# Optimization experiments

Measured on AMD Instinct MI355X. Metric: run time of the kernel, lower is better.

Reference implementation:

```python
import jax, jax.numpy as jnp
import numpy as np

H = 12        # num attention heads
W = 256       # one-sided window (attention_window // 2)
NEG = -1e9    # additive mask value


def setup_inputs() -> dict:
    key = jax.random.key(0)
    ks = jax.random.split(key, 6)
    B, S, D = 2, 4096, 768
    inp = {
        "hidden_states": jax.random.normal(ks[0], (B, S, D), dtype=jnp.float32),
        "attention_mask": jnp.zeros((B, S), dtype=jnp.float32),
        "Wq": jax.random.normal(ks[1], (D, D), dtype=jnp.float32) * 0.02,
        "bq": jnp.zeros((D,), dtype=jnp.float32),
        "Wk": jax.random.normal(ks[2], (D, D), dtype=jnp.float32) * 0.02,
        "bk": jnp.zeros((D,), dtype=jnp.float32),
        "Wv": jax.random.normal(ks[3], (D, D), dtype=jnp.float32) * 0.02,
        "bv": jnp.zeros((D,), dtype=jnp.float32),
        "Wo": jax.random.normal(ks[4], (D, D), dtype=jnp.float32) * 0.02,
        "bo": jnp.zeros((D,), dtype=jnp.float32),
    }
    return inp


def _sliding_window_attn(hidden_states, attention_mask, Wq, bq, Wk, bk, Wv, bv, Wo, bo):
    B, S, D = hidden_states.shape
    dh = D // H
    b = W                 # chunk size == one-sided window
    nb = S // b           # number of chunks (S must be multiple of W)

    # projections; Longformer scales the query by 1/sqrt(d_head)
    q = (hidden_states @ Wq.T + bq) / jnp.sqrt(jnp.float32(dh))
    k = hidden_states @ Wk.T + bk
    v = hidden_states @ Wv.T + bv

    # [B, H, S, dh]
    q = q.reshape(B, S, H, dh).transpose(0, 2, 1, 3)
    k = k.reshape(B, S, H, dh).transpose(0, 2, 1, 3)
    v = v.reshape(B, S, H, dh).transpose(0, 2, 1, 3)

    # chunk queries: [B, H, nb, b, dh]
    qb = q.reshape(B, H, nb, b, dh)

    # pad K/V by one chunk on each side, gather 3 consecutive chunks per query chunk
    kp = jnp.pad(k, ((0, 0), (0, 0), (b, b), (0, 0)))
    vp = jnp.pad(v, ((0, 0), (0, 0), (b, b), (0, 0)))
    idx = jnp.arange(nb)[:, None] * b + jnp.arange(3 * b)[None, :]  # [nb, 3b] into padded seq
    kw = kp[:, :, idx]  # [B, H, nb, 3b, dh]
    vw = vp[:, :, idx]  # [B, H, nb, 3b, dh]

    # banded scores: [B, H, nb, b, 3b]
    scores = jnp.einsum("bhnqd,bhnkd->bhnqk", qb, kw)

    # band mask: query at local pos qi (global n*b+qi) vs key at local pos ki
    # (global n*b + ki - b); relative offset = ki - b - qi, keep |offset| <= W
    rel = jnp.arange(3 * b)[None, :] - b - jnp.arange(b)[:, None]      # [b, 3b]
    band = jnp.abs(rel) <= W
    # sequence-boundary mask: key global position must lie in [0, S)
    kpos = idx - b                                                      # [nb, 3b]
    inbounds = (kpos >= 0) & (kpos < S)
    valid = band[None, :, :] & inbounds[:, None, :]                     # [nb, b, 3b]

    # key padding bias from attention_mask (wrapper passes attention_mask * -1)
    neg_mask = attention_mask * -1.0                                    # [B, S]
    mp = jnp.pad(neg_mask, ((0, 0), (b, b)))
    key_bias = mp[:, idx]                                               # [B, nb, 3b]

    scores = scores + key_bias[:, None, :, None, :]
    scores = jnp.where(valid[None, None], scores, NEG)

    probs = jax.nn.softmax(scores, axis=-1)
    ctx = jnp.einsum("bhnqk,bhnkd->bhnqd", probs, vw)                   # [B, H, nb, b, dh]
    ctx = ctx.reshape(B, H, S, dh).transpose(0, 2, 1, 3).reshape(B, S, D)

    return ctx @ Wo.T + bo


def reference(hidden_states, attention_mask, Wq, bq, Wk, bk, Wv, bv, Wo, bo):
    return _sliding_window_attn(hidden_states, attention_mask,
                                Wq, bq, Wk, bk, Wv, bv, Wo, bo)
```

## Files before the change

kernel.cpp:

```cpp
#include <hip/hip_runtime.h>
#include <hip/hip_bf16.h>
#include <stdint.h>

#define NH 12
#define DH 64
#define SEQ 4096
#define DM 768
#define NEGV -1e9f
#define LOG2E 1.4426950408889634f
#define QSCALE 0.1803368801111601f

using bf16x8 = __attribute__((ext_vector_type(8))) short;
using f32x4  = __attribute__((ext_vector_type(4))) float;

static __device__ __forceinline__ short f2bf(float f) {
  unsigned u = __builtin_bit_cast(unsigned, f);
  u += 0x7fffu + ((u >> 16) & 1u);
  return (short)(u >> 16);
}

static __device__ __forceinline__ unsigned pack2bf(float lo, float hi) {
  unsigned a = __builtin_bit_cast(unsigned, lo);
  a += 0x7fffu + ((a >> 16) & 1u);
  unsigned b = __builtin_bit_cast(unsigned, hi);
  b += 0x7fffu + ((b >> 16) & 1u);
  return (a >> 16) | (b & 0xffff0000u);
}

static __device__ __forceinline__ void gload16(const void* g, void* l) {
  __builtin_amdgcn_global_load_lds(
      (const __attribute__((address_space(1))) unsigned*)g,
      (__attribute__((address_space(3))) unsigned*)l, 16, 0, 0);
}

static __device__ __forceinline__ f32x4 mfma16(bf16x8 a, bf16x8 b, f32x4 c) {
  return __builtin_amdgcn_mfma_f32_16x16x32_bf16(a, b, c, 0, 0, 0);
}

#define SBAR() __builtin_amdgcn_sched_barrier(0)
#define WAIT8() asm volatile("s_waitcnt vmcnt(8)" ::: "memory")
#define WAIT4() asm volatile("s_waitcnt vmcnt(4)" ::: "memory")
#define WAIT0() asm volatile("s_waitcnt vmcnt(0)" ::: "memory")
#define HBAR() __builtin_amdgcn_s_barrier()

__global__ __launch_bounds__(256) void cvt_x(const float* __restrict__ X,
                                             short* __restrict__ Xb, int n4) {
  int i = blockIdx.x * 256 + threadIdx.x;
  if (i >= n4) return;
  float4 v = ((const float4*)X)[i];
  short4 o; o.x = f2bf(v.x); o.y = f2bf(v.y); o.z = f2bf(v.z); o.w = f2bf(v.w);
  ((short4*)Xb)[i] = o;
}

__global__ __launch_bounds__(256) void cvt_w(
    const float* __restrict__ Wq, const float* __restrict__ Wk,
    const float* __restrict__ Wv, const float* __restrict__ Wo,
    short* __restrict__ Wqkv, short* __restrict__ Wob) {
  int i = blockIdx.x * 256 + threadIdx.x;
  const int n1 = 2304 * 768 / 4;
  if (i < n1) {
    int e = i * 4;
    int row = e / 768;
    const float* src;
    float sc = 1.0f;
    if (row < 768)       { src = Wq + e; sc = QSCALE; }
    else if (row < 1536) { src = Wk + e - 768 * 768; }
    else                 { src = Wv + e - 1536 * 768; }
    float4 v = *(const float4*)src;
    short4 o; o.x = f2bf(v.x * sc); o.y = f2bf(v.y * sc);
    o.z = f2bf(v.z * sc); o.w = f2bf(v.w * sc);
    ((short4*)Wqkv)[i] = o;
  } else {
    int j = i - n1;
    if (j >= 768 * 768 / 4) return;
    float4 v = ((const float4*)Wo)[j];
    short4 o; o.x = f2bf(v.x); o.y = f2bf(v.y); o.z = f2bf(v.z); o.w = f2bf(v.w);
    ((short4*)Wob)[j] = o;
  }
}

#define GEMM_PIPELINE(SM, AG, BG, ACC, LANE, WR, WC)                           \
  {                                                                            \
    const int l15 = (LANE) & 15, gw = (LANE) >> 4;                             \
    const int s_ = (l15 >> 1) & 3;                                             \
    const int fcol = ((gw ^ s_) << 3);                                         \
    const int NT = 24;                                             \
    auto stage = [&](int t) {                                                  \
      short* ab = (SM) + ((t & 3) << 12);                                      \
      short* bb = (SM) + 16384 + ((t & 3) << 12);                              \
      int kt = t << 5;                                                         \
      gload16((AG) + kt, ab + ldst);                                           \
      gload16((AG) + kt + 64 * 768, ab + ldst + 2048);                         \
      gload16((BG) + kt, bb + ldst);                                           \
      gload16((BG) + kt + 64 * 768, bb + ldst + 2048);                         \
    };                                                                         \
    auto compute = [&](int t) {                                                \
      const short* ab = (SM) + ((t & 3) << 12);                                \
      const short* bb = (SM) + 16384 + ((t & 3) << 12);                        \
      bf16x8 af[4], bf[4];                                                     \
      _Pragma("unroll") for (int mi = 0; mi < 4; ++mi)                         \
          af[mi] = *(const bf16x8*)(ab + ((WR) + mi * 16 + l15) * 32 + fcol);  \
      _Pragma("unroll") for (int ni = 0; ni < 4; ++ni)                         \
          bf[ni] = *(const bf16x8*)(bb + ((WC) + ni * 16 + l15) * 32 + fcol);  \
      __builtin_amdgcn_s_setprio(1);                                           \
      _Pragma("unroll") for (int mi = 0; mi < 4; ++mi)                         \
          _Pragma("unroll") for (int ni = 0; ni < 4; ++ni)                     \
              ACC[mi][ni] = mfma16(af[mi], bf[ni], ACC[mi][ni]);               \
      __builtin_amdgcn_s_setprio(0);                                           \
    };                                                                         \
    stage(0); stage(1); stage(2);                                              \
    SBAR();                                                                    \
    _Pragma("unroll 1") for (int i = 0; i < NT - 3; ++i) {                     \
      SBAR(); WAIT8(); HBAR(); SBAR();                                         \
      stage(i + 3);                                                            \
      SBAR();                                                                  \
      compute(i);                                                              \
    }                                                                          \
    SBAR(); WAIT8(); HBAR(); SBAR(); compute(NT - 3);                          \
    SBAR(); WAIT4(); HBAR(); SBAR(); compute(NT - 2);                          \
    SBAR(); WAIT0(); HBAR(); SBAR(); compute(NT - 1);                          \
  }

__global__ __launch_bounds__(256) void gemm_qkv(
    const short* __restrict__ Xb, const short* __restrict__ Wqkv,
    const float* __restrict__ bq, const float* __restrict__ bk,
    const float* __restrict__ bv,
    short* __restrict__ qO, short* __restrict__ kO, short* __restrict__ vT) {
  __shared__ __align__(16) short sm[32768];
  const int tid = threadIdx.x, lane = tid & 63, wid = tid >> 6;
  const int xcd = blockIdx.x & 7, kk = blockIdx.x >> 3;
  const int m0 = (xcd * 8 + (kk & 7)) * 128;
  const int n0 = (kk >> 3) * 128;
  const int wr = (wid >> 1) * 64, wc = (wid & 1) * 64;
  const int srow = tid >> 2;
  const int scol = (((tid & 3) ^ ((srow >> 1) & 3)) << 3);
  const short* Ag = Xb + (m0 + srow) * 768 + scol;
  const short* Bg = Wqkv + (n0 + srow) * 768 + scol;
  const int ldst = tid * 8;

  const int src = n0 / 768;
  const int nloc = n0 % 768;
  float bias[4];
#pragma unroll
  for (int ni = 0; ni < 4; ++ni) {
    int c = nloc + wc + ni * 16 + (lane & 15);
    bias[ni] = (src == 0) ? bq[c] * QSCALE : (src == 1) ? bk[c] : bv[c];
  }
  WAIT0(); SBAR();

  f32x4 acc[4][4] = {};
  GEMM_PIPELINE(sm, Ag, Bg, acc, lane, wr, wc);

  const int bb = m0 >> 12;
  const int s0 = m0 & (SEQ - 1);
  __syncthreads();
  if (src < 2) {
#pragma unroll
    for (int mi = 0; mi < 4; ++mi)
#pragma unroll
      for (int ni = 0; ni < 4; ++ni) {
        int row = wr + mi * 16 + ((lane >> 4) << 2);
        int col = wc + ni * 16 + (lane & 15);
#pragma unroll
        for (int r = 0; r < 4; ++r)
          sm[(row + r) * 132 + col] = f2bf(acc[mi][ni][r] + bias[ni]);
      }
    __syncthreads();
    short* dst = (src == 0) ? qO : kO;
    for (int u = tid; u < 8192; u += 256) {
      int r = u >> 6, cp = (u & 63) << 1;
      unsigned val = *(const unsigned*)&sm[r * 132 + cp];
      int c = nloc + cp;
      int h = c >> 6, d = c & 63;
      *(unsigned*)&dst[(((bb * NH + h) * SEQ) + s0 + r) * DH + d] = val;
    }
  } else {
#pragma unroll
    for (int mi = 0; mi < 4; ++mi)
#pragma unroll
      for (int ni = 0; ni < 4; ++ni) {
        int row = wr + mi * 16 + ((lane >> 4) << 2);
        int col = wc + ni * 16 + (lane & 15);
        short4 pk;
        pk.x = f2bf(acc[mi][ni][0] + bias[ni]);
        pk.y = f2bf(acc[mi][ni][1] + bias[ni]);
        pk.z = f2bf(acc[mi][ni][2] + bias[ni]);
        pk.w = f2bf(acc[mi][ni][3] + bias[ni]);
        *(short4*)&sm[col * 132 + row] = pk;
      }
    __syncthreads();
    for (int u = tid; u < 8192; u += 256) {
      int cc = u >> 6, rp = (u & 63) << 1;
      unsigned val = *(const unsigned*)&sm[cc * 132 + rp];
      int c = nloc + cc;
      int h = c >> 6, d = c & 63;
      *(unsigned*)&vT[(((bb * NH + h) * DH) + d) * SEQ + s0 + rp] = val;
    }
  }
}

__global__ __launch_bounds__(512, 4) void attn(
    const short* __restrict__ qI, const short* __restrict__ kI,
    const short* __restrict__ vT, const float* __restrict__ amask,
    short* __restrict__ ctx) {
  __shared__ __align__(16) short Ks[128 * 64];
  __shared__ __align__(16) short Vs[64 * 128];
  __shared__ __align__(16) short Ps[8][16 * 132];
  const int tid = threadIdx.x, lane = tid & 63, wid = tid >> 6;
  const int vb_id = (blockIdx.x & 7) * 96 + (blockIdx.x >> 3);
  const int strip = vb_id & 31;
  const int hh = (vb_id >> 5) % 12;
  const int bb = vb_id / 384;
  const int s0 = strip * 128;
  const int n = s0 >> 8;
  const int i0 = s0 & 255;
  const int bh = bb * NH + hh;
  const int m = lane & 15, hq = lane >> 4;
  const int swz = m & 7;
  const int iw = i0 + (wid << 4);

  const short* qbase = qI + ((size_t)(bh * SEQ) + s0 + (wid << 4)) * DH;
  const bf16x8 aq0 = *(const bf16x8*)(qbase + m * DH + (hq << 3));
  const bf16x8 aq1 = *(const bf16x8*)(qbase + m * DH + 32 + (hq << 3));

  const int kb_s0 = m * 64 + ((hq ^ swz) << 3);
  const int kb_s1 = m * 64 + (((hq + 4) ^ swz) << 3);
  const int vk0 = m * 128 + ((hq ^ swz) << 3);
  const int vk1 = m * 128 + (((hq + 4) ^ swz) << 3);
  const int vk2 = m * 128 + (((hq + 8) ^ swz) << 3);
  const int vk3 = m * 128 + (((hq + 12) ^ swz) << 3);
  short* Pw = Ps[wid];
  const int pwr = m * 132;

  const int e0 = tid * 8, e1 = tid * 8 + 4096;
  const int kj0 = e0 >> 6, kj1 = e1 >> 6;
  const int ksrc0 = kj0 * DH + ((((e0 >> 3) & 7) ^ (kj0 & 7)) << 3);
  const int ksrc1 = kj1 * DH + ((((e1 >> 3) & 7) ^ (kj1 & 7)) << 3);
  const int vd0 = e0 >> 7, vd1 = e1 >> 7;
  const int vsrc0 = vd0 * SEQ + ((((e0 >> 3) & 15) ^ (vd0 & 7)) << 3);
  const int vsrc1 = vd1 * SEQ + ((((e1 >> 3) & 15) ^ (vd1 & 7)) << 3);

  const short* kg0 = kI + (size_t)bh * SEQ * DH;
  const short* vg0 = vT + (size_t)bh * DH * SEQ;
  const float* mk0 = amask + bb * SEQ + (hq << 2);

  f32x4 acc[4] = {};
  float mrow = -1e30f, lrow = 0.f;

#pragma unroll 1
  for (int c = 0; c < 6; ++c) {
    const int j0 = c << 7;
    const int kpos0 = ((n - 1) << 8) + j0;
    if (kpos0 < 0 || kpos0 >= SEQ) continue;
    if (j0 + 127 < i0 || j0 > i0 + 639) continue;

    __syncthreads();
    {
      const short* kb = kg0 + (size_t)kpos0 * DH;
      gload16(kb + ksrc0, (short*)Ks + e0);
      gload16(kb + ksrc1, (short*)Ks + e1);
      const short* vbp = vg0 + kpos0;
      gload16(vbp + vsrc0, (short*)Vs + e0);
      gload16(vbp + vsrc1, (short*)Vs + e1);
    }
    __syncthreads();

    f32x4 sc[8];
    __builtin_amdgcn_s_setprio(1);
#pragma unroll
    for (int jt = 0; jt < 8; ++jt) {
      bf16x8 k0 = *(const bf16x8*)(Ks + jt * 1024 + kb_s0);
      bf16x8 k1 = *(const bf16x8*)(Ks + jt * 1024 + kb_s1);
      f32x4 z = {};
      z = mfma16(k0, aq0, z);
      z = mfma16(k1, aq1, z);
      sc[jt] = z;
    }
    __builtin_amdgcn_s_setprio(0);

    const float* mp = mk0 + kpos0;
    float mn = mrow;
    const bool interior = (j0 >= iw + 15) && (j0 <= iw + 385);
    if (interior) {
#pragma unroll
      for (int jt = 0; jt < 8; ++jt) {
        float4 b4 = *(const float4*)(mp + jt * 16);
#pragma unroll
        for (int r = 0; r < 4; ++r) {
          float s = fmaf(-LOG2E, (&b4.x)[r], sc[jt][r]);
          sc[jt][r] = s;
          mn = fmaxf(mn, s);
        }
      }
    } else {
      const int iq = iw + m;
#pragma unroll
      for (int jt = 0; jt < 8; ++jt) {
        float4 b4 = *(const float4*)(mp + jt * 16);
        const int jb = j0 + jt * 16 + (hq << 2);
#pragma unroll
        for (int r = 0; r < 4; ++r) {
          int j = jb + r;
          float s = fmaf(-LOG2E, (&b4.x)[r], sc[jt][r]);
          s = (j >= iq && j <= iq + 512) ? s : NEGV;
          sc[jt][r] = s;
          mn = fmaxf(mn, s);
        }
      }
    }
    mn = fmaxf(mn, __shfl_xor(mn, 16));
    mn = fmaxf(mn, __shfl_xor(mn, 32));

    float l0 = 0.f;
#pragma unroll
    for (int jt = 0; jt < 8; ++jt) {
      float p0 = exp2f(sc[jt][0] - mn);
      float p1 = exp2f(sc[jt][1] - mn);
      float p2 = exp2f(sc[jt][2] - mn);
      float p3 = exp2f(sc[jt][3] - mn);
      l0 += (p0 + p1) + (p2 + p3);
      uint2 u;
      u.x = pack2bf(p0, p1);
      u.y = pack2bf(p2, p3);
      *(uint2*)(Pw + pwr + jt * 16 + (hq << 2)) = u;
    }
    l0 += __shfl_xor(l0, 16);
    l0 += __shfl_xor(l0, 32);
    const float scl = exp2f(mrow - mn);
    lrow = lrow * scl + l0;
    mrow = mn;
    const float s0r = __shfl(scl, (hq << 2) + 0);
    const float s1r = __shfl(scl, (hq << 2) + 1);
    const float s2r = __shfl(scl, (hq << 2) + 2);
    const float s3r = __shfl(scl, (hq << 2) + 3);
#pragma unroll
    for (int nt = 0; nt < 4; ++nt) {
      acc[nt][0] *= s0r; acc[nt][1] *= s1r;
      acc[nt][2] *= s2r; acc[nt][3] *= s3r;
    }

    asm volatile("s_waitcnt lgkmcnt(0)" ::: "memory");
    __builtin_amdgcn_sched_barrier(0);

    __builtin_amdgcn_s_setprio(1);
#pragma unroll
    for (int ks = 0; ks < 4; ++ks) {
      bf16x8 pa = *(const bf16x8*)(Pw + pwr + ks * 32 + (hq << 3));
      const int vkk = (ks == 0) ? vk0 : (ks == 1) ? vk1 : (ks == 2) ? vk2 : vk3;
#pragma unroll
      for (int nt = 0; nt < 4; ++nt) {
        bf16x8 vv = *(const bf16x8*)(Vs + nt * 2048 + vkk);
        acc[nt] = mfma16(pa, vv, acc[nt]);
      }
    }
    __builtin_amdgcn_s_setprio(0);
  }

  const float inv = 1.0f / lrow;
  const float i0r = __shfl(inv, (hq << 2) + 0);
  const float i1r = __shfl(inv, (hq << 2) + 1);
  const float i2r = __shfl(inv, (hq << 2) + 2);
  const float i3r = __shfl(inv, (hq << 2) + 3);
#pragma unroll
  for (int nt = 0; nt < 4; ++nt) {
    Pw[((hq << 2) + 0) * 72 + nt * 16 + m] = f2bf(acc[nt][0] * i0r);
    Pw[((hq << 2) + 1) * 72 + nt * 16 + m] = f2bf(acc[nt][1] * i1r);
    Pw[((hq << 2) + 2) * 72 + nt * 16 + m] = f2bf(acc[nt][2] * i2r);
    Pw[((hq << 2) + 3) * 72 + nt * 16 + m] = f2bf(acc[nt][3] * i3r);
  }
  asm volatile("s_waitcnt lgkmcnt(0)" ::: "memory");
  __builtin_amdgcn_sched_barrier(0);
#pragma unroll
  for (int it = 0; it < 2; ++it) {
    int row = it * 8 + (lane >> 3);
    bf16x8 val = *(const bf16x8*)(Pw + row * 72 + ((lane & 7) << 3));
    *(bf16x8*)(ctx + ((size_t)(bb * SEQ) + s0 + (wid << 4) + row) * DM +
               hh * DH + ((lane & 7) << 3)) = val;
  }
}

__global__ __launch_bounds__(256) void gemm_out(
    const short* __restrict__ Cb, const short* __restrict__ Wob,
    const float* __restrict__ bo, float* __restrict__ out) {
  __shared__ __align__(16) short sm[32768];
  const int tid = threadIdx.x, lane = tid & 63, wid = tid >> 6;
  const int xcd = blockIdx.x & 7, kk = blockIdx.x >> 3;
  const int m0 = (xcd * 8 + (kk & 7)) * 128;
  const int n0 = (kk >> 3) * 128;
  const int wr = (wid >> 1) * 64, wc = (wid & 1) * 64;
  const int srow = tid >> 2;
  const int scol = (((tid & 3) ^ ((srow >> 1) & 3)) << 3);
  const short* Ag = Cb + (m0 + srow) * 768 + scol;
  const short* Bg = Wob + (n0 + srow) * 768 + scol;
  const int ldst = tid * 8;

  float bias[4];
#pragma unroll
  for (int ni = 0; ni < 4; ++ni)
    bias[ni] = bo[n0 + wc + ni * 16 + (lane & 15)];
  WAIT0(); SBAR();

  f32x4 acc[4][4] = {};
  GEMM_PIPELINE(sm, Ag, Bg, acc, lane, wr, wc);

#pragma unroll
  for (int mi = 0; mi < 4; ++mi)
#pragma unroll
    for (int ni = 0; ni < 4; ++ni) {
      int row = m0 + wr + mi * 16 + ((lane >> 4) << 2);
      int col = n0 + wc + ni * 16 + (lane & 15);
#pragma unroll
      for (int r = 0; r < 4; ++r)
        out[(row + r) * DM + col] = acc[mi][ni][r] + bias[ni];
    }
}

extern "C" void kernel_launch(void* const* d_in, const int* in_sizes, int n_in,
                              void* d_out, int out_size, void* d_ws, size_t ws_size,
                              hipStream_t stream) {
  (void)in_sizes; (void)n_in; (void)out_size; (void)ws_size;
  const float* hs    = (const float*)d_in[0];
  const float* amask = (const float*)d_in[1];
  const float* Wq = (const float*)d_in[2];
  const float* bq = (const float*)d_in[3];
  const float* Wk = (const float*)d_in[4];
  const float* bk = (const float*)d_in[5];
  const float* Wv = (const float*)d_in[6];
  const float* bv = (const float*)d_in[7];
  const float* Wo = (const float*)d_in[8];
  const float* bo = (const float*)d_in[9];
  float* out = (float*)d_out;
  char* ws = (char*)d_ws;
  short* Xb   = (short*)(ws);
  short* Wqkv = (short*)(ws + 12582912);
  short* Wob  = (short*)(ws + 16121856);
  short* qB   = (short*)(ws + 17301504);
  short* kB   = (short*)(ws + 29884416);
  short* vTB  = (short*)(ws + 42467328);
  short* ctx  = Xb;

  cvt_x<<<dim3(6144), dim3(256), 0, stream>>>(hs, Xb, 8192 * 768 / 4);
  cvt_w<<<dim3(2304), dim3(256), 0, stream>>>(Wq, Wk, Wv, Wo, Wqkv, Wob);
  gemm_qkv<<<dim3(1152), dim3(256), 0, stream>>>(Xb, Wqkv, bq, bk, bv, qB, kB, vTB);
  attn<<<dim3(768), dim3(512), 0, stream>>>(qB, kB, vTB, amask, ctx);
  gemm_out<<<dim3(384), dim3(256), 0, stream>>>(ctx, Wob, bo, out);
}
```

Baseline: 134.8 us.

## Prefetch next K/V chunk into registers, stage mask in LDS, lazy softmax rescale

Replaces the per-chunk global_load_lds with a register prefetch. The next K/V chunk is loaded into registers during the current chunk's QK compute and then written to LDS behind barriers, so global latency overlaps with math. The attention-mask bias for the whole window is staged once into shared memory instead of being read from global each chunk. The chunk loop bounds are computed directly rather than skipped with continue. Online-softmax rescaling is skipped when the running max grows by at most 4 (log2 units), which saves exp and shuffle work but risks larger intermediate values in bf16 P.

```diff
diff --git a/kernel.cpp b/kernel.cpp
--- a/kernel.cpp
+++ b/kernel.cpp
@@ -41,6 +41,7 @@
 #define WAIT8() asm volatile("s_waitcnt vmcnt(8)" ::: "memory")
 #define WAIT4() asm volatile("s_waitcnt vmcnt(4)" ::: "memory")
 #define WAIT0() asm volatile("s_waitcnt vmcnt(0)" ::: "memory")
+#define LKWAIT() asm volatile("s_waitcnt lgkmcnt(0)" ::: "memory")
 #define HBAR() __builtin_amdgcn_s_barrier()
 
 __global__ __launch_bounds__(256) void cvt_x(const float* __restrict__ X,
@@ -206,6 +207,7 @@
   __shared__ __align__(16) short Ks[128 * 64];
   __shared__ __align__(16) short Vs[64 * 128];
   __shared__ __align__(16) short Ps[8][16 * 132];
+  __shared__ __align__(16) float BiasL[768];
   const int tid = threadIdx.x, lane = tid & 63, wid = tid >> 6;
   const int vb_id = (blockIdx.x & 7) * 96 + (blockIdx.x >> 3);
   const int strip = vb_id & 31;
@@ -214,6 +216,7 @@
   const int s0 = strip * 128;
   const int n = s0 >> 8;
   const int i0 = s0 & 255;
+  const int base = (n - 1) * 256;
   const int bh = bb * NH + hh;
   const int m = lane & 15, hq = lane >> 4;
   const int swz = m & 7;
@@ -242,28 +245,42 @@
 
   const short* kg0 = kI + (size_t)bh * SEQ * DH;
   const short* vg0 = vT + (size_t)bh * DH * SEQ;
-  const float* mk0 = amask + bb * SEQ + (hq << 2);
+
+  if (tid < 192) {
+    int idx = base + tid * 4;
+    idx = idx < 0 ? 0 : (idx > SEQ - 4 ? SEQ - 4 : idx);
+    float4 bv = *(const float4*)(amask + bb * SEQ + idx);
+    *(float4*)&BiasL[tid * 4] = bv;
+  }
+
+  int cl0 = (n == 0) ? 2 : 0;
+  if (i0 == 128 && cl0 < 1) cl0 = 1;
+  int chi = (i0 == 0) ? 4 : 5;
+  if (n == 15) chi = 3;
+
+  uint4 rk0, rk1, rv0, rv1;
+  {
+    const int kpos0 = base + (cl0 << 7);
+    const short* kb = kg0 + (size_t)kpos0 * DH;
+    rk0 = *(const uint4*)(kb + ksrc0);
+    rk1 = *(const uint4*)(kb + ksrc1);
+    const short* vbp = vg0 + kpos0;
+    rv0 = *(const uint4*)(vbp + vsrc0);
+    rv1 = *(const uint4*)(vbp + vsrc1);
+  }
 
   f32x4 acc[4] = {};
   float mrow = -1e30f, lrow = 0.f;
 
 #pragma unroll 1
-  for (int c = 0; c < 6; ++c) {
-    const int j0 = c << 7;
-    const int kpos0 = ((n - 1) << 8) + j0;
-    if (kpos0 < 0 || kpos0 >= SEQ) continue;
-    if (j0 + 127 < i0 || j0 > i0 + 639) continue;
-
-    __syncthreads();
-    {
-      const short* kb = kg0 + (size_t)kpos0 * DH;
-      gload16(kb + ksrc0, (short*)Ks + e0);
-      gload16(kb + ksrc1, (short*)Ks + e1);
-      const short* vbp = vg0 + kpos0;
-      gload16(vbp + vsrc0, (short*)Vs + e0);
-      gload16(vbp + vsrc1, (short*)Vs + e1);
-    }
-    __syncthreads();
+  for (int cc = cl0; cc <= chi; ++cc) {
+    const int j0 = cc << 7;
+    SBAR(); LKWAIT(); HBAR(); SBAR();
+    *(uint4*)((short*)Ks + e0) = rk0;
+    *(uint4*)((short*)Ks + e1) = rk1;
+    *(uint4*)((short*)Vs + e0) = rv0;
+    *(uint4*)((short*)Vs + e1) = rv1;
+    SBAR(); LKWAIT(); HBAR(); SBAR();
 
     f32x4 sc[8];
     __builtin_amdgcn_s_setprio(1);
@@ -278,13 +295,23 @@
     }
     __builtin_amdgcn_s_setprio(0);
 
-    const float* mp = mk0 + kpos0;
+    if (cc < chi) {
+      const int kposn = base + ((cc + 1) << 7);
+      const short* kb = kg0 + (size_t)kposn * DH;
+      rk0 = *(const uint4*)(kb + ksrc0);
+      rk1 = *(const uint4*)(kb + ksrc1);
+      const short* vbp = vg0 + kposn;
+      rv0 = *(const uint4*)(vbp + vsrc0);
+      rv1 = *(const uint4*)(vbp + vsrc1);
+    }
+
     float mn = mrow;
     const bool interior = (j0 >= iw + 15) && (j0 <= iw + 385);
+    const float* bl = BiasL + j0 + (hq << 2);
     if (interior) {
 #pragma unroll
       for (int jt = 0; jt < 8; ++jt) {
-        float4 b4 = *(const float4*)(mp + jt * 16);
+        float4 b4 = *(const float4*)(bl + jt * 16);
 #pragma unroll
         for (int r = 0; r < 4; ++r) {
           float s = fmaf(-LOG2E, (&b4.x)[r], sc[jt][r]);
@@ -296,7 +323,7 @@
       const int iq = iw + m;
 #pragma unroll
       for (int jt = 0; jt < 8; ++jt) {
-        float4 b4 = *(const float4*)(mp + jt * 16);
+        float4 b4 = *(const float4*)(bl + jt * 16);
         const int jb = j0 + jt * 16 + (hq << 2);
 #pragma unroll
         for (int r = 0; r < 4; ++r) {
@@ -311,13 +338,16 @@
     mn = fmaxf(mn, __shfl_xor(mn, 16));
     mn = fmaxf(mn, __shfl_xor(mn, 32));
 
+    const bool resc = !__all(mn - mrow <= 4.0f);
+    const float mbase = resc ? mn : mrow;
+
     float l0 = 0.f;
 #pragma unroll
     for (int jt = 0; jt < 8; ++jt) {
-      float p0 = exp2f(sc[jt][0] - mn);
-      float p1 = exp2f(sc[jt][1] - mn);
-      float p2 = exp2f(sc[jt][2] - mn);
-      float p3 = exp2f(sc[jt][3] - mn);
+      float p0 = exp2f(sc[jt][0] - mbase);
+      float p1 = exp2f(sc[jt][1] - mbase);
+      float p2 = exp2f(sc[jt][2] - mbase);
+      float p3 = exp2f(sc[jt][3] - mbase);
       l0 += (p0 + p1) + (p2 + p3);
       uint2 u;
       u.x = pack2bf(p0, p1);
@@ -326,21 +356,24 @@
     }
     l0 += __shfl_xor(l0, 16);
     l0 += __shfl_xor(l0, 32);
-    const float scl = exp2f(mrow - mn);
-    lrow = lrow * scl + l0;
-    mrow = mn;
-    const float s0r = __shfl(scl, (hq << 2) + 0);
-    const float s1r = __shfl(scl, (hq << 2) + 1);
-    const float s2r = __shfl(scl, (hq << 2) + 2);
-    const float s3r = __shfl(scl, (hq << 2) + 3);
-#pragma unroll
-    for (int nt = 0; nt < 4; ++nt) {
-      acc[nt][0] *= s0r; acc[nt][1] *= s1r;
-      acc[nt][2] *= s2r; acc[nt][3] *= s3r;
-    }
-
-    asm volatile("s_waitcnt lgkmcnt(0)" ::: "memory");
-    __builtin_amdgcn_sched_barrier(0);
+    if (resc) {
+      const float scl = exp2f(mrow - mn);
+      lrow = lrow * scl + l0;
+      mrow = mn;
+      const float s0r = __shfl(scl, (hq << 2) + 0);
+      const float s1r = __shfl(scl, (hq << 2) + 1);
+      const float s2r = __shfl(scl, (hq << 2) + 2);
+      const float s3r = __shfl(scl, (hq << 2) + 3);
+#pragma unroll
+      for (int nt = 0; nt < 4; ++nt) {
+        acc[nt][0] *= s0r; acc[nt][1] *= s1r;
+        acc[nt][2] *= s2r; acc[nt][3] *= s3r;
+      }
+    } else {
+      lrow += l0;
+    }
+
+    LKWAIT(); SBAR();
 
     __builtin_amdgcn_s_setprio(1);
 #pragma unroll
@@ -368,8 +401,7 @@
     Pw[((hq << 2) + 2) * 72 + nt * 16 + m] = f2bf(acc[nt][2] * i2r);
     Pw[((hq << 2) + 3) * 72 + nt * 16 + m] = f2bf(acc[nt][3] * i3r);
   }
-  asm volatile("s_waitcnt lgkmcnt(0)" ::: "memory");
-  __builtin_amdgcn_sched_barrier(0);
+  LKWAIT(); SBAR();
 #pragma unroll
   for (int it = 0; it < 2; ++it) {
     int row = it * 8 + (lane >> 3);
```

After: 145.0 us. +7.6%, slower.

## Load K/V tiles directly from global per wave, dropping shared staging and block barriers

Applied to the files above, without the earlier changes.

The attention kernel no longer stages K and V tiles into shared memory with block-wide barriers. Each wave now reads its K and V fragments straight from global memory (relying on L1/L2 for reuse across the 8 waves) and skips chunks per wave using the wave's own query range instead of the block's. This removes the two __syncthreads per chunk and frees LDS, and the occupancy hint is dropped. In exchange every wave issues redundant global loads with less coalescing and exposed latency before each MFMA.

```diff
diff --git a/kernel.cpp b/kernel.cpp
--- a/kernel.cpp
+++ b/kernel.cpp
@@ -41,6 +41,7 @@
 #define WAIT8() asm volatile("s_waitcnt vmcnt(8)" ::: "memory")
 #define WAIT4() asm volatile("s_waitcnt vmcnt(4)" ::: "memory")
 #define WAIT0() asm volatile("s_waitcnt vmcnt(0)" ::: "memory")
+#define LKWAIT() asm volatile("s_waitcnt lgkmcnt(0)" ::: "memory")
 #define HBAR() __builtin_amdgcn_s_barrier()
 
 __global__ __launch_bounds__(256) void cvt_x(const float* __restrict__ X,
@@ -199,12 +200,10 @@
   }
 }
 
-__global__ __launch_bounds__(512, 4) void attn(
+__global__ __launch_bounds__(512) void attn(
     const short* __restrict__ qI, const short* __restrict__ kI,
     const short* __restrict__ vT, const float* __restrict__ amask,
     short* __restrict__ ctx) {
-  __shared__ __align__(16) short Ks[128 * 64];
-  __shared__ __align__(16) short Vs[64 * 128];
   __shared__ __align__(16) short Ps[8][16 * 132];
   const int tid = threadIdx.x, lane = tid & 63, wid = tid >> 6;
   const int vb_id = (blockIdx.x & 7) * 96 + (blockIdx.x >> 3);
@@ -214,31 +213,20 @@
   const int s0 = strip * 128;
   const int n = s0 >> 8;
   const int i0 = s0 & 255;
+  const int base = (n - 1) * 256;
   const int bh = bb * NH + hh;
   const int m = lane & 15, hq = lane >> 4;
-  const int swz = m & 7;
   const int iw = i0 + (wid << 4);
 
   const short* qbase = qI + ((size_t)(bh * SEQ) + s0 + (wid << 4)) * DH;
   const bf16x8 aq0 = *(const bf16x8*)(qbase + m * DH + (hq << 3));
   const bf16x8 aq1 = *(const bf16x8*)(qbase + m * DH + 32 + (hq << 3));
 
-  const int kb_s0 = m * 64 + ((hq ^ swz) << 3);
-  const int kb_s1 = m * 64 + (((hq + 4) ^ swz) << 3);
-  const int vk0 = m * 128 + ((hq ^ swz) << 3);
-  const int vk1 = m * 128 + (((hq + 4) ^ swz) << 3);
-  const int vk2 = m * 128 + (((hq + 8) ^ swz) << 3);
-  const int vk3 = m * 128 + (((hq + 12) ^ swz) << 3);
   short* Pw = Ps[wid];
   const int pwr = m * 132;
 
-  const int e0 = tid * 8, e1 = tid * 8 + 4096;
-  const int kj0 = e0 >> 6, kj1 = e1 >> 6;
-  const int ksrc0 = kj0 * DH + ((((e0 >> 3) & 7) ^ (kj0 & 7)) << 3);
-  const int ksrc1 = kj1 * DH + ((((e1 >> 3) & 7) ^ (kj1 & 7)) << 3);
-  const int vd0 = e0 >> 7, vd1 = e1 >> 7;
-  const int vsrc0 = vd0 * SEQ + ((((e0 >> 3) & 15) ^ (vd0 & 7)) << 3);
-  const int vsrc1 = vd1 * SEQ + ((((e1 >> 3) & 15) ^ (vd1 & 7)) << 3);
+  const int koff = m * DH + (hq << 3);
+  const int voff = m * SEQ + (hq << 3);
 
   const short* kg0 = kI + (size_t)bh * SEQ * DH;
   const short* vg0 = vT + (size_t)bh * DH * SEQ;
@@ -250,33 +238,21 @@
 #pragma unroll 1
   for (int c = 0; c < 6; ++c) {
     const int j0 = c << 7;
-    const int kpos0 = ((n - 1) << 8) + j0;
+    const int kpos0 = base + j0;
     if (kpos0 < 0 || kpos0 >= SEQ) continue;
-    if (j0 + 127 < i0 || j0 > i0 + 639) continue;
-
-    __syncthreads();
-    {
-      const short* kb = kg0 + (size_t)kpos0 * DH;
-      gload16(kb + ksrc0, (short*)Ks + e0);
-      gload16(kb + ksrc1, (short*)Ks + e1);
-      const short* vbp = vg0 + kpos0;
-      gload16(vbp + vsrc0, (short*)Vs + e0);
-      gload16(vbp + vsrc1, (short*)Vs + e1);
-    }
-    __syncthreads();
-
+    if (j0 + 127 < iw || j0 > iw + 527) continue;
+
+    const short* kb = kg0 + (size_t)kpos0 * DH + koff;
     f32x4 sc[8];
-    __builtin_amdgcn_s_setprio(1);
 #pragma unroll
     for (int jt = 0; jt < 8; ++jt) {
-      bf16x8 k0 = *(const bf16x8*)(Ks + jt * 1024 + kb_s0);
-      bf16x8 k1 = *(const bf16x8*)(Ks + jt * 1024 + kb_s1);
+      bf16x8 k0 = *(const bf16x8*)(kb + jt * 1024);
+      bf16x8 k1 = *(const bf16x8*)(kb + jt * 1024 + 32);
       f32x4 z = {};
       z = mfma16(k0, aq0, z);
       z = mfma16(k1, aq1, z);
       sc[jt] = z;
     }
-    __builtin_amdgcn_s_setprio(0);
 
     const float* mp = mk0 + kpos0;
     float mn = mrow;
@@ -339,21 +315,18 @@
       acc[nt][2] *= s2r; acc[nt][3] *= s3r;
     }
 
-    asm volatile("s_waitcnt lgkmcnt(0)" ::: "memory");
-    __builtin_amdgcn_sched_barrier(0);
-
-    __builtin_amdgcn_s_setprio(1);
+    LKWAIT(); SBAR();
+
+    const short* vb = vg0 + kpos0 + voff;
 #pragma unroll
     for (int ks = 0; ks < 4; ++ks) {
       bf16x8 pa = *(const bf16x8*)(Pw + pwr + ks * 32 + (hq << 3));
-      const int vkk = (ks == 0) ? vk0 : (ks == 1) ? vk1 : (ks == 2) ? vk2 : vk3;
 #pragma unroll
       for (int nt = 0; nt < 4; ++nt) {
-        bf16x8 vv = *(const bf16x8*)(Vs + nt * 2048 + vkk);
+        bf16x8 vv = *(const bf16x8*)(vb + nt * 16 * SEQ + ks * 32);
         acc[nt] = mfma16(pa, vv, acc[nt]);
       }
     }
-    __builtin_amdgcn_s_setprio(0);
   }
 
   const float inv = 1.0f / lrow;
@@ -368,8 +341,7 @@
     Pw[((hq << 2) + 2) * 72 + nt * 16 + m] = f2bf(acc[nt][2] * i2r);
     Pw[((hq << 2) + 3) * 72 + nt * 16 + m] = f2bf(acc[nt][3] * i3r);
   }
-  asm volatile("s_waitcnt lgkmcnt(0)" ::: "memory");
-  __builtin_amdgcn_sched_barrier(0);
+  LKWAIT(); SBAR();
 #pragma unroll
   for (int it = 0; it < 2; ++it) {
     int row = it * 8 + (lane >> 3);
```

Result: slower. 202.3 us (+50.1%).

## Switch GEMM pipeline to double-buffered BK=64 tiles with fewer barriers

Applied to the files above, without the earlier changes.

The shared bf16 GEMM pipeline used by the QKV and output projections now loads 64-wide K tiles into two LDS buffers instead of 32-wide tiles into a four-deep ring. The loop count halves to 12, each compute step issues two MFMA sub-steps, and the LDS swizzle and global-load mapping are changed to match 64-element rows. The aim is to halve barrier and wait overhead per K step and issue larger loads. In exchange, prefetch depth drops from three stages to one, and the loop adds a second barrier per iteration before restaging.

```diff
diff --git a/kernel.cpp b/kernel.cpp
--- a/kernel.cpp
+++ b/kernel.cpp
@@ -39,7 +39,6 @@
 
 #define SBAR() __builtin_amdgcn_sched_barrier(0)
 #define WAIT8() asm volatile("s_waitcnt vmcnt(8)" ::: "memory")
-#define WAIT4() asm volatile("s_waitcnt vmcnt(4)" ::: "memory")
 #define WAIT0() asm volatile("s_waitcnt vmcnt(0)" ::: "memory")
 #define HBAR() __builtin_amdgcn_s_barrier()
 
@@ -83,42 +82,47 @@
   {                                                                            \
     const int l15 = (LANE) & 15, gw = (LANE) >> 4;                             \
     const int s_ = (l15 >> 1) & 3;                                             \
-    const int fcol = ((gw ^ s_) << 3);                                         \
-    const int NT = 24;                                             \
+    const int NT = 12;                                             \
     auto stage = [&](int t) {                                                  \
-      short* ab = (SM) + ((t & 3) << 12);                                      \
-      short* bb = (SM) + 16384 + ((t & 3) << 12);                              \
-      int kt = t << 5;                                                         \
+      short* ab = (SM) + ((t & 1) << 13);                                      \
+      short* bb = (SM) + 16384 + ((t & 1) << 13);                              \
+      int kt = t << 6;                                                         \
       gload16((AG) + kt, ab + ldst);                                           \
-      gload16((AG) + kt + 64 * 768, ab + ldst + 2048);                         \
+      gload16((AG) + kt + 32 * 768, ab + ldst + 2048);                         \
+      gload16((AG) + kt + 64 * 768, ab + ldst + 4096);                         \
+      gload16((AG) + kt + 96 * 768, ab + ldst + 6144);                         \
       gload16((BG) + kt, bb + ldst);                                           \
-      gload16((BG) + kt + 64 * 768, bb + ldst + 2048);                         \
+      gload16((BG) + kt + 32 * 768, bb + ldst + 2048);                         \
+      gload16((BG) + kt + 64 * 768, bb + ldst + 4096);                         \
+      gload16((BG) + kt + 96 * 768, bb + ldst + 6144);                         \
     };                                                                         \
     auto compute = [&](int t) {                                                \
-      const short* ab = (SM) + ((t & 3) << 12);                                \
-      const short* bb = (SM) + 16384 + ((t & 3) << 12);                        \
-      bf16x8 af[4], bf[4];                                                     \
-      _Pragma("unroll") for (int mi = 0; mi < 4; ++mi)                         \
-          af[mi] = *(const bf16x8*)(ab + ((WR) + mi * 16 + l15) * 32 + fcol);  \
-      _Pragma("unroll") for (int ni = 0; ni < 4; ++ni)                         \
-          bf[ni] = *(const bf16x8*)(bb + ((WC) + ni * 16 + l15) * 32 + fcol);  \
-      __builtin_amdgcn_s_setprio(1);                                           \
-      _Pragma("unroll") for (int mi = 0; mi < 4; ++mi)                         \
-          _Pragma("unroll") for (int ni = 0; ni < 4; ++ni)                     \
-              ACC[mi][ni] = mfma16(af[mi], bf[ni], ACC[mi][ni]);               \
-      __builtin_amdgcn_s_setprio(0);                                           \
+      const short* ab = (SM) + ((t & 1) << 13);                                \
+      const short* bb = (SM) + 16384 + ((t & 1) << 13);                        \
+      _Pragma("unroll") for (int kk = 0; kk < 2; ++kk) {                       \
+        const int fc = (((kk << 2) + (gw ^ s_)) << 3);                         \
+        bf16x8 af[4], bf[4];                                                   \
+        _Pragma("unroll") for (int mi = 0; mi < 4; ++mi)                       \
+            af[mi] = *(const bf16x8*)(ab + ((WR) + mi * 16 + l15) * 64 + fc);  \
+        _Pragma("unroll") for (int ni = 0; ni < 4; ++ni)                       \
+            bf[ni] = *(const bf16x8*)(bb + ((WC) + ni * 16 + l15) * 64 + fc);  \
+        __builtin_amdgcn_s_setprio(1);                                         \
+        _Pragma("unroll") for (int mi = 0; mi < 4; ++mi)                       \
+            _Pragma("unroll") for (int ni = 0; ni < 4; ++ni)                   \
+                ACC[mi][ni] = mfma16(af[mi], bf[ni], ACC[mi][ni]);             \
+        __builtin_amdgcn_s_setprio(0);                                         \
+      }                                                                        \
     };                                                                         \
-    stage(0); stage(1); stage(2);                                              \
+    stage(0); stage(1);                                                        \
     SBAR();                                                                    \
-    _Pragma("unroll 1") for (int i = 0; i < NT - 3; ++i) {                     \
-      SBAR(); WAIT8(); HBAR(); SBAR();                                         \
-      stage(i + 3);                                                            \
+    _Pragma("unroll 1") for (int i = 0; i < NT; ++i) {                         \
       SBAR();                                                                  \
+      if (i < NT - 1) { WAIT8(); } else { WAIT0(); }                           \
+      HBAR(); SBAR();                                                          \
       compute(i);                                                              \
+      SBAR(); HBAR();                                                          \
+      if (i + 2 < NT) stage(i + 2);                                            \
     }                                                                          \
-    SBAR(); WAIT8(); HBAR(); SBAR(); compute(NT - 3);                          \
-    SBAR(); WAIT4(); HBAR(); SBAR(); compute(NT - 2);                          \
-    SBAR(); WAIT0(); HBAR(); SBAR(); compute(NT - 1);                          \
   }
 
 __global__ __launch_bounds__(256) void gemm_qkv(
@@ -132,8 +136,8 @@
   const int m0 = (xcd * 8 + (kk & 7)) * 128;
   const int n0 = (kk >> 3) * 128;
   const int wr = (wid >> 1) * 64, wc = (wid & 1) * 64;
-  const int srow = tid >> 2;
-  const int scol = (((tid & 3) ^ ((srow >> 1) & 3)) << 3);
+  const int srow = tid >> 3;
+  const int scol = (((tid & 7) ^ ((tid >> 4) & 3)) << 3);
   const short* Ag = Xb + (m0 + srow) * 768 + scol;
   const short* Bg = Wqkv + (n0 + srow) * 768 + scol;
   const int ldst = tid * 8;
@@ -388,8 +392,8 @@
   const int m0 = (xcd * 8 + (kk & 7)) * 128;
   const int n0 = (kk >> 3) * 128;
   const int wr = (wid >> 1) * 64, wc = (wid & 1) * 64;
-  const int srow = tid >> 2;
-  const int scol = (((tid & 3) ^ ((srow >> 1) & 3)) << 3);
+  const int srow = tid >> 3;
+  const int scol = (((tid & 7) ^ ((tid >> 4) & 3)) << 3);
   const short* Ag = Cb + (m0 + srow) * 768 + scol;
   const short* Bg = Wob + (n0 + srow) * 768 + scol;
   const int ldst = tid * 8;
```

Result: faster. 131.4 us (-2.5%).
